# Kernel optimization log

Hardware: AMD Instinct MI355X
Metric: run time of the kernel (lower is better)

Reference implementation:

```python
import jax, jax.numpy as jnp
import numpy as np

N_NODES = 100000
N_EDGES = 1200000
N_GRAPHS = 128
IN_C, HID_C, OUT_C = 64, 128, 16


def setup_inputs() -> dict:
    key = jax.random.key(0)
    ks = jax.random.split(key, 6)
    x = jax.random.normal(ks[0], (N_NODES, IN_C), dtype=jnp.float32)
    edge_index = jax.random.randint(ks[1], (2, N_EDGES), 0, N_NODES, dtype=jnp.int64)
    batch = jnp.sort(jax.random.randint(ks[2], (N_NODES,), 0, N_GRAPHS, dtype=jnp.int64))
    W1 = jax.random.normal(ks[3], (IN_C, HID_C), dtype=jnp.float32) * (1.0 / np.sqrt(IN_C))
    b1 = jnp.zeros((HID_C,), jnp.float32)
    W2 = jax.random.normal(ks[4], (HID_C, OUT_C), dtype=jnp.float32) * (1.0 / np.sqrt(HID_C))
    b2 = jnp.zeros((OUT_C,), jnp.float32)
    return {"x": x, "edge_index": edge_index, "batch": batch,
            "W1": W1, "b1": b1, "W2": W2, "b2": b2}


def gcn_conv(x, src, dst, W, b, n):
    """PyG GCNConv: add self-loops, symmetric deg^{-1/2} normalization, scatter-add."""
    h = x @ W                                   # [n, out] dense transform first
    loop = jnp.arange(n, dtype=src.dtype)
    s = jnp.concatenate([src, loop])            # edges + self-loops
    d = jnp.concatenate([dst, loop])
    deg = jax.ops.segment_sum(jnp.ones(d.shape[0], h.dtype), d, num_segments=n)
    dinv = jnp.where(deg > 0, jax.lax.rsqrt(deg), jnp.zeros((), h.dtype))
    norm = dinv[s] * dinv[d]                    # [E + n]
    msg = h[s] * norm[:, None]                  # gather + scale
    return jax.ops.segment_sum(msg, d, num_segments=n) + b  # scatter-add


def reference(x, edge_index, batch, W1, b1, W2, b2):
    n = x.shape[0]
    src, dst = edge_index[0], edge_index[1]
    h = jax.nn.relu(gcn_conv(x, src, dst, W1, b1, n))
    h = gcn_conv(h, src, dst, W2, b2, n)
    # global_mean_pool over batch ids
    sums = jax.ops.segment_sum(h, batch, num_segments=N_GRAPHS)
    cnts = jax.ops.segment_sum(jnp.ones((n,), h.dtype), batch, num_segments=N_GRAPHS)
    pooled = sums / jnp.maximum(cnts, 1.0)[:, None]   # [N_GRAPHS, OUT_C]
    return jax.nn.log_softmax(pooled, axis=1)
```

## Files before the change

kernel.cpp:

```cpp
#include <hip/hip_runtime.h>
#include <hip/hip_bf16.h>


#define THREADS 256
#define NPB 256
#define BSTRIDE 4096
#define CH 4096
#define NBMAX 512

typedef __attribute__((ext_vector_type(8))) short bf16x8;
typedef __attribute__((ext_vector_type(4))) float f32x4;

__device__ __forceinline__ float bfu_lo(unsigned int u) {
    union { unsigned int i; float f; } v; v.i = u << 16; return v.f;
}
__device__ __forceinline__ float bfu_hi(unsigned int u) {
    union { unsigned int i; float f; } v; v.i = u & 0xffff0000u; return v.f;
}
__device__ __forceinline__ unsigned short f2bf(float f) {
    union { float f; unsigned int i; } v; v.f = f;
    unsigned int r = v.i + 0x7fff + ((v.i >> 16) & 1);
    return (unsigned short)(r >> 16);
}
__device__ __forceinline__ unsigned int packbf(float lo, float hi) {
    return (unsigned int)f2bf(lo) | ((unsigned int)f2bf(hi) << 16);
}
__device__ __forceinline__ void unpack8(uint4 u, float* f) {
    f[0] = bfu_lo(u.x); f[1] = bfu_hi(u.x);
    f[2] = bfu_lo(u.y); f[3] = bfu_hi(u.y);
    f[4] = bfu_lo(u.z); f[5] = bfu_hi(u.z);
    f[6] = bfu_lo(u.w); f[7] = bfu_hi(u.w);
}

__global__ __launch_bounds__(THREADS) void k_partition(const int* __restrict__ src,
                                                       const int* __restrict__ dst,
                                                       int* __restrict__ bucketCursor,
                                                       unsigned int* __restrict__ ebuf,
                                                       int E, int NB) {
    __shared__ int h[NBMAX];
    __shared__ int base[NBMAX];
    __shared__ int cnt[NBMAX];
    for (int b = threadIdx.x; b < NBMAX; b += THREADS) { h[b] = 0; cnt[b] = 0; }
    __syncthreads();
    int b0 = blockIdx.x * CH;
    for (int k = 0; k < CH; k += THREADS) {
        int e = b0 + k + threadIdx.x;
        if (e < E) atomicAdd(&h[dst[e] >> 8], 1);
    }
    __syncthreads();
    for (int b = threadIdx.x; b < NB; b += THREADS)
        if (h[b]) base[b] = b * BSTRIDE + atomicAdd(&bucketCursor[b], h[b]);
    __syncthreads();
    for (int k = 0; k < CH; k += THREADS) {
        int e = b0 + k + threadIdx.x;
        if (e < E) {
            int s = src[e], d = dst[e];
            int b = d >> 8;
            int i = base[b] + atomicAdd(&cnt[b], 1);
            ebuf[i] = ((unsigned int)(d & (NPB - 1)) << 17) | (unsigned int)s;
        }
    }
}

__global__ __launch_bounds__(THREADS) void k_bucket_csr(const unsigned int* __restrict__ ebuf,
                                                        const int* __restrict__ bucketCursor,
                                                        const float* __restrict__ x,
                                                        int* __restrict__ offs,
                                                        int* __restrict__ deg,
                                                        int* __restrict__ srcs,
                                                        float* __restrict__ dinv,
                                                        uint4* __restrict__ xnb,
                                                        int n) {
    __shared__ unsigned int eL[BSTRIDE];
    __shared__ int c[NPB];
    __shared__ int cur[NPB];
    __shared__ float dloc[NPB];
    __shared__ int sh[THREADS];
    const int tid = threadIdx.x;
    const int b = blockIdx.x;
    const int nbase = b * NPB;
    const int w0 = b * BSTRIDE;
    const int cnt_b = bucketCursor[b];
    c[tid] = 0;
    __syncthreads();
    for (int i = tid; i < cnt_b; i += THREADS) {
        unsigned int e = ebuf[w0 + i];
        eL[i] = e;
        atomicAdd(&c[e >> 17], 1);
    }
    __syncthreads();
    int c0 = c[tid];
    sh[tid] = c0;
    __syncthreads();
    for (int step = 1; step < THREADS; step <<= 1) {
        int t = (tid >= step) ? sh[tid - step] : 0;
        __syncthreads();
        sh[tid] += t;
        __syncthreads();
    }
    int excl = sh[tid] - c0;
    int node = nbase + tid;
    float dv = rsqrtf((float)(c0 + 1));
    dloc[tid] = dv;
    if (node < n) {
        offs[node] = w0 + excl;
        deg[node] = c0;
        dinv[node] = dv;
    }
    cur[tid] = excl;
    __syncthreads();
    for (int i = tid; i < cnt_b; i += THREADS) {
        unsigned int e = eL[i];
        int pos = w0 + atomicAdd(&cur[e >> 17], 1);
        srcs[pos] = (int)(e & 0x1FFFFu);
    }
    const float4* X4 = (const float4*)x;
    for (int i = tid; i < NPB * 8; i += THREADS) {
        int ln = i >> 3;
        int node2 = nbase + ln;
        if (node2 >= n) break;
        int q = i & 7;
        float dd = dloc[ln];
        float4 a = X4[(size_t)node2 * 16 + q * 2];
        float4 bb = X4[(size_t)node2 * 16 + q * 2 + 1];
        uint4 o;
        o.x = packbf(a.x * dd, a.y * dd);
        o.y = packbf(a.z * dd, a.w * dd);
        o.z = packbf(bb.x * dd, bb.y * dd);
        o.w = packbf(bb.z * dd, bb.w * dd);
        xnb[(size_t)node2 * 8 + q] = o;
    }
}

__global__ __launch_bounds__(THREADS) void k_gather1(const int* __restrict__ offs,
                                                     const int* __restrict__ deg,
                                                     const int* __restrict__ srcs,
                                                     const float* __restrict__ dinv,
                                                     const uint4* __restrict__ xnb,
                                                     uint4* __restrict__ aggb, int n) {
    int idx = blockIdx.x * THREADS + threadIdx.x;
    int node = idx >> 3;
    if (node >= n) return;
    int q = idx & 7;
    float acc[8];
    unpack8(xnb[(size_t)node * 8 + q], acc);
    int e0 = offs[node], e1 = e0 + deg[node];
    for (int e = e0; e < e1; ++e) {
        int s = srcs[e];
        float t[8];
        unpack8(xnb[(size_t)s * 8 + q], t);
#pragma unroll
        for (int j = 0; j < 8; ++j) acc[j] += t[j];
    }
    float dd = dinv[node];
    uint4 o;
    o.x = packbf(acc[0] * dd, acc[1] * dd);
    o.y = packbf(acc[2] * dd, acc[3] * dd);
    o.z = packbf(acc[4] * dd, acc[5] * dd);
    o.w = packbf(acc[6] * dd, acc[7] * dd);
    aggb[(size_t)node * 8 + q] = o;
}

__global__ __launch_bounds__(THREADS) void k_gemm12m(const unsigned short* __restrict__ aggb,
                                                     const float* __restrict__ W1,
                                                     const float* __restrict__ b1,
                                                     const float* __restrict__ W2,
                                                     const float* __restrict__ dinv,
                                                     unsigned short* __restrict__ ts,
                                                     int n, int ntiles) {
    __shared__ unsigned short h1L[4][16][136];
    const int wave = threadIdx.x >> 6;
    const int lane = threadIdx.x & 63;
    const int col = lane & 15;
    const int ko = lane >> 4;

    bf16x8 bfr1[2][8];
#pragma unroll
    for (int ks = 0; ks < 2; ++ks)
#pragma unroll
        for (int nt = 0; nt < 8; ++nt) {
            bf16x8 b;
#pragma unroll
            for (int j = 0; j < 8; ++j)
                b[j] = (short)f2bf(W1[(ks * 32 + ko * 8 + j) * 128 + nt * 16 + col]);
            bfr1[ks][nt] = b;
        }
    float bias[8];
#pragma unroll
    for (int nt = 0; nt < 8; ++nt) bias[nt] = b1[nt * 16 + col];
    bf16x8 bfr2[4];
#pragma unroll
    for (int ks = 0; ks < 4; ++ks) {
        bf16x8 b;
#pragma unroll
        for (int j = 0; j < 8; ++j)
            b[j] = (short)f2bf(W2[(ks * 32 + ko * 8 + j) * 16 + col]);
        bfr2[ks] = b;
    }

    const int tile0 = (blockIdx.x * 4 + wave) * 4;
    for (int t = 0; t < 4; ++t) {
        int tile = tile0 + t;
        if (tile >= ntiles) return;
        int r0 = tile * 16;
        int rowA = r0 + col;
        if (rowA >= n) rowA = n - 1;
        const bf16x8* Ap = (const bf16x8*)(aggb + (size_t)rowA * 64 + ko * 8);
        bf16x8 a0 = Ap[0];
        bf16x8 a1 = Ap[4];
        f32x4 acc[8];
#pragma unroll
        for (int nt = 0; nt < 8; ++nt) acc[nt] = (f32x4){0.f, 0.f, 0.f, 0.f};
#pragma unroll
        for (int nt = 0; nt < 8; ++nt) {
            acc[nt] = __builtin_amdgcn_mfma_f32_16x16x32_bf16(a0, bfr1[0][nt], acc[nt], 0, 0, 0);
            acc[nt] = __builtin_amdgcn_mfma_f32_16x16x32_bf16(a1, bfr1[1][nt], acc[nt], 0, 0, 0);
        }
#pragma unroll
        for (int nt = 0; nt < 8; ++nt)
#pragma unroll
            for (int r = 0; r < 4; ++r)
                h1L[wave][ko * 4 + r][nt * 16 + col] = f2bf(fmaxf(acc[nt][r] + bias[nt], 0.f));
        f32x4 acc2 = (f32x4){0.f, 0.f, 0.f, 0.f};
#pragma unroll
        for (int ks = 0; ks < 4; ++ks) {
            bf16x8 a2 = *(const bf16x8*)&h1L[wave][col][ks * 32 + ko * 8];
            acc2 = __builtin_amdgcn_mfma_f32_16x16x32_bf16(a2, bfr2[ks], acc2, 0, 0, 0);
        }
#pragma unroll
        for (int r = 0; r < 4; ++r) {
            int row = r0 + ko * 4 + r;
            if (row < n) {
                float dd = dinv[row];
                ts[(size_t)row * 16 + col] = f2bf(acc2[r] * dd);
            }
        }
    }
}

__global__ __launch_bounds__(THREADS) void k_gather2(const int* __restrict__ offs,
                                                     const int* __restrict__ deg,
                                                     const int* __restrict__ srcs,
                                                     const float* __restrict__ dinv,
                                                     const uint4* __restrict__ ts,
                                                     float* __restrict__ h2, int n) {
    int idx = blockIdx.x * THREADS + threadIdx.x;
    int node = idx >> 1;
    if (node >= n) return;
    int q = idx & 1;
    float acc[8];
    unpack8(ts[(size_t)node * 2 + q], acc);
    int e0 = offs[node], e1 = e0 + deg[node];
    for (int e = e0; e < e1; ++e) {
        int s = srcs[e];
        float t[8];
        unpack8(ts[(size_t)s * 2 + q], t);
#pragma unroll
        for (int j = 0; j < 8; ++j) acc[j] += t[j];
    }
    float dd = dinv[node];
    float4 o0 = {acc[0] * dd, acc[1] * dd, acc[2] * dd, acc[3] * dd};
    float4 o1 = {acc[4] * dd, acc[5] * dd, acc[6] * dd, acc[7] * dd};
    float4* O = (float4*)(h2 + (size_t)node * 16 + q * 8);
    O[0] = o0;
    O[1] = o1;
}

__global__ __launch_bounds__(THREADS) void k_poolfinal(const float* __restrict__ h2,
                                                       const int* __restrict__ batch,
                                                       const float* __restrict__ b2,
                                                       float* __restrict__ out, int n) {
    int g = blockIdx.x;
    int lo = 0, hi = n;
    while (lo < hi) { int mid = (lo + hi) >> 1; if (batch[mid] < g) lo = mid + 1; else hi = mid; }
    int s0 = lo;
    hi = n;
    while (lo < hi) { int mid = (lo + hi) >> 1; if (batch[mid] < g + 1) lo = mid + 1; else hi = mid; }
    int s1 = lo;

    int c = threadIdx.x & 15;
    int rg = threadIdx.x >> 4;
    float acc = 0.f;
    for (int i = s0 + rg; i < s1; i += 16) acc += h2[(size_t)i * 16 + c];
    __shared__ float red[THREADS];
    red[threadIdx.x] = acc;
    __syncthreads();
    for (int step = 128; step >= 16; step >>= 1) {
        if (threadIdx.x < step) red[threadIdx.x] += red[threadIdx.x + step];
        __syncthreads();
    }
    if (threadIdx.x == 0) {
        float cnt = fmaxf((float)(s1 - s0), 1.0f);
        float v[16];
        float mx = -1e30f;
#pragma unroll
        for (int k = 0; k < 16; ++k) {
            v[k] = red[k] / cnt + b2[k];
            mx = fmaxf(mx, v[k]);
        }
        float se = 0.f;
#pragma unroll
        for (int k = 0; k < 16; ++k) se += expf(v[k] - mx);
        float lse = logf(se) + mx;
#pragma unroll
        for (int k = 0; k < 16; ++k) out[g * 16 + k] = v[k] - lse;
    }
}

extern "C" void kernel_launch(void* const* d_in, const int* in_sizes, int n_in,
                              void* d_out, int out_size, void* d_ws, size_t ws_size,
                              hipStream_t stream) {
    const float* x    = (const float*)d_in[0];
    const int* edges  = (const int*)d_in[1];
    const int* batch  = (const int*)d_in[2];
    const float* W1   = (const float*)d_in[3];
    const float* b1   = (const float*)d_in[4];
    const float* W2   = (const float*)d_in[5];
    const float* b2   = (const float*)d_in[6];
    float* out        = (float*)d_out;

    const int n = in_sizes[2];
    const int E = in_sizes[1] / 2;
    const int* src = edges;
    const int* dst = edges + E;
    const int NB = (n + NPB - 1) / NPB;
    const int npart = (E + CH - 1) / CH;
    const int ntiles = (n + 15) / 16;

    char* ws = (char*)d_ws;
    size_t off = 0;
    auto carve = [&](size_t bytes) { char* p = ws + off; off = (off + bytes + 255) & ~(size_t)255; return p; };
    int*   bucketCursor = (int*)carve(NBMAX * 4);
    int*   offs    = (int*)carve((size_t)n * 4);
    int*   deg     = (int*)carve((size_t)n * 4);
    int*   srcs    = (int*)carve((size_t)NB * BSTRIDE * 4);
    float* dinv    = (float*)carve((size_t)n * 4);
    uint4* xnb     = (uint4*)carve((size_t)n * 64 * 2);
    char*  aggreg  = (char*)carve((size_t)n * 64 * 2);
    char*  big     = (char*)carve((size_t)NB * BSTRIDE * 4 > (size_t)n * 128 * 2
                                  ? (size_t)NB * BSTRIDE * 4 : (size_t)n * 128 * 2);
    unsigned int* ebuf = (unsigned int*)big;
    unsigned short* ts = (unsigned short*)big;
    unsigned short* aggb = (unsigned short*)aggreg;
    float* h2 = (float*)(aggreg + (size_t)n * 16 * 4);

    auto blks = [](long long work) { return (int)((work + THREADS - 1) / THREADS); };

    hipMemsetAsync(bucketCursor, 0, NBMAX * 4, stream);
    k_partition  <<<npart, THREADS, 0, stream>>>(src, dst, bucketCursor, ebuf, E, NB);
    k_bucket_csr <<<NB, THREADS, 0, stream>>>(ebuf, bucketCursor, x, offs, deg, srcs, dinv, xnb, n);

    k_gather1 <<<blks((long long)n * 8), THREADS, 0, stream>>>(offs, deg, srcs, dinv, xnb, (uint4*)aggb, n);
    k_gemm12m <<<(ntiles + 15) / 16, THREADS, 0, stream>>>(aggb, W1, b1, W2, dinv, ts, n, ntiles);
    k_gather2 <<<blks((long long)n * 2), THREADS, 0, stream>>>(offs, deg, srcs, dinv, (const uint4*)ts, h2, n);

    k_poolfinal <<<128, THREADS, 0, stream>>>(h2, batch, b2, out, n);
}
```

Baseline: 132.6 us.

## Fuse second-layer gather with mean pooling via shared-memory atomics; cache dst in LDS

The second GCN aggregation now pools directly into per-graph sums. Each block accumulates into a shared-memory table with atomics and then flushes it to global sums, so the per-node h2 array is never written or re-read, and a tiny single-block kernel does the normalisation and log-softmax. The partition kernel also keeps dst values in LDS so they are read from global memory only once. This costs shared-memory atomic contention and global float atomics, which make the summation order nondeterministic.

```diff
diff --git a/kernel.cpp b/kernel.cpp
--- a/kernel.cpp
+++ b/kernel.cpp
@@ -7,6 +7,7 @@
 #define BSTRIDE 4096
 #define CH 4096
 #define NBMAX 512
+#define NGRAPH 128
 
 typedef __attribute__((ext_vector_type(8))) short bf16x8;
 typedef __attribute__((ext_vector_type(4))) float f32x4;
@@ -40,12 +41,17 @@
     __shared__ int h[NBMAX];
     __shared__ int base[NBMAX];
     __shared__ int cnt[NBMAX];
+    __shared__ int dL[CH];
     for (int b = threadIdx.x; b < NBMAX; b += THREADS) { h[b] = 0; cnt[b] = 0; }
     __syncthreads();
     int b0 = blockIdx.x * CH;
     for (int k = 0; k < CH; k += THREADS) {
         int e = b0 + k + threadIdx.x;
-        if (e < E) atomicAdd(&h[dst[e] >> 8], 1);
+        if (e < E) {
+            int d = dst[e];
+            dL[k + threadIdx.x] = d;
+            atomicAdd(&h[d >> 8], 1);
+        }
     }
     __syncthreads();
     for (int b = threadIdx.x; b < NB; b += THREADS)
@@ -54,7 +60,8 @@
     for (int k = 0; k < CH; k += THREADS) {
         int e = b0 + k + threadIdx.x;
         if (e < E) {
-            int s = src[e], d = dst[e];
+            int s = src[e];
+            int d = dL[k + threadIdx.x];
             int b = d >> 8;
             int i = base[b] + atomicAdd(&cnt[b], 1);
             ebuf[i] = ((unsigned int)(d & (NPB - 1)) << 17) | (unsigned int)s;
@@ -238,73 +245,69 @@
     }
 }
 
-__global__ __launch_bounds__(THREADS) void k_gather2(const int* __restrict__ offs,
-                                                     const int* __restrict__ deg,
-                                                     const int* __restrict__ srcs,
-                                                     const float* __restrict__ dinv,
-                                                     const uint4* __restrict__ ts,
-                                                     float* __restrict__ h2, int n) {
-    int idx = blockIdx.x * THREADS + threadIdx.x;
+__global__ __launch_bounds__(THREADS) void k_gatherpool(const int* __restrict__ offs,
+                                                        const int* __restrict__ deg,
+                                                        const int* __restrict__ srcs,
+                                                        const float* __restrict__ dinv,
+                                                        const uint4* __restrict__ ts,
+                                                        const int* __restrict__ batch,
+                                                        float* __restrict__ sums, int n) {
+    __shared__ float gsum[NGRAPH * 16];
+    const int tid = threadIdx.x;
+    for (int i = tid; i < NGRAPH * 16; i += THREADS) gsum[i] = 0.f;
+    __syncthreads();
+    int idx = blockIdx.x * THREADS + tid;
     int node = idx >> 1;
-    if (node >= n) return;
-    int q = idx & 1;
-    float acc[8];
-    unpack8(ts[(size_t)node * 2 + q], acc);
-    int e0 = offs[node], e1 = e0 + deg[node];
-    for (int e = e0; e < e1; ++e) {
-        int s = srcs[e];
-        float t[8];
-        unpack8(ts[(size_t)s * 2 + q], t);
-#pragma unroll
-        for (int j = 0; j < 8; ++j) acc[j] += t[j];
-    }
-    float dd = dinv[node];
-    float4 o0 = {acc[0] * dd, acc[1] * dd, acc[2] * dd, acc[3] * dd};
-    float4 o1 = {acc[4] * dd, acc[5] * dd, acc[6] * dd, acc[7] * dd};
-    float4* O = (float4*)(h2 + (size_t)node * 16 + q * 8);
-    O[0] = o0;
-    O[1] = o1;
-}
-
-__global__ __launch_bounds__(THREADS) void k_poolfinal(const float* __restrict__ h2,
-                                                       const int* __restrict__ batch,
-                                                       const float* __restrict__ b2,
-                                                       float* __restrict__ out, int n) {
-    int g = blockIdx.x;
+    if (node < n) {
+        int q = idx & 1;
+        float acc[8];
+        unpack8(ts[(size_t)node * 2 + q], acc);
+        int e0 = offs[node], e1 = e0 + deg[node];
+        for (int e = e0; e < e1; ++e) {
+            int s = srcs[e];
+            float t[8];
+            unpack8(ts[(size_t)s * 2 + q], t);
+#pragma unroll
+            for (int j = 0; j < 8; ++j) acc[j] += t[j];
+        }
+        float dd = dinv[node];
+        int g = batch[node];
+        float* row = &gsum[g * 16 + q * 8];
+#pragma unroll
+        for (int j = 0; j < 8; ++j) atomicAdd(&row[j], acc[j] * dd);
+    }
+    __syncthreads();
+    for (int i = tid; i < NGRAPH * 16; i += THREADS) {
+        float v = gsum[i];
+        if (v != 0.f) atomicAdd(&sums[i], v);
+    }
+}
+
+__global__ __launch_bounds__(NGRAPH) void k_final(const float* __restrict__ sums,
+                                                  const int* __restrict__ batch,
+                                                  const float* __restrict__ b2,
+                                                  float* __restrict__ out, int n) {
+    int g = threadIdx.x;
     int lo = 0, hi = n;
     while (lo < hi) { int mid = (lo + hi) >> 1; if (batch[mid] < g) lo = mid + 1; else hi = mid; }
     int s0 = lo;
     hi = n;
     while (lo < hi) { int mid = (lo + hi) >> 1; if (batch[mid] < g + 1) lo = mid + 1; else hi = mid; }
     int s1 = lo;
-
-    int c = threadIdx.x & 15;
-    int rg = threadIdx.x >> 4;
-    float acc = 0.f;
-    for (int i = s0 + rg; i < s1; i += 16) acc += h2[(size_t)i * 16 + c];
-    __shared__ float red[THREADS];
-    red[threadIdx.x] = acc;
-    __syncthreads();
-    for (int step = 128; step >= 16; step >>= 1) {
-        if (threadIdx.x < step) red[threadIdx.x] += red[threadIdx.x + step];
-        __syncthreads();
-    }
-    if (threadIdx.x == 0) {
-        float cnt = fmaxf((float)(s1 - s0), 1.0f);
-        float v[16];
-        float mx = -1e30f;
-#pragma unroll
-        for (int k = 0; k < 16; ++k) {
-            v[k] = red[k] / cnt + b2[k];
-            mx = fmaxf(mx, v[k]);
-        }
-        float se = 0.f;
-#pragma unroll
-        for (int k = 0; k < 16; ++k) se += expf(v[k] - mx);
-        float lse = logf(se) + mx;
-#pragma unroll
-        for (int k = 0; k < 16; ++k) out[g * 16 + k] = v[k] - lse;
-    }
+    float cnt = fmaxf((float)(s1 - s0), 1.0f);
+    float v[16];
+    float mx = -1e30f;
+#pragma unroll
+    for (int c = 0; c < 16; ++c) {
+        v[c] = sums[g * 16 + c] / cnt + b2[c];
+        mx = fmaxf(mx, v[c]);
+    }
+    float se = 0.f;
+#pragma unroll
+    for (int c = 0; c < 16; ++c) se += expf(v[c] - mx);
+    float lse = logf(se) + mx;
+#pragma unroll
+    for (int c = 0; c < 16; ++c) out[g * 16 + c] = v[c] - lse;
 }
 
 extern "C" void kernel_launch(void* const* d_in, const int* in_sizes, int n_in,
@@ -331,6 +334,7 @@
     size_t off = 0;
     auto carve = [&](size_t bytes) { char* p = ws + off; off = (off + bytes + 255) & ~(size_t)255; return p; };
     int*   bucketCursor = (int*)carve(NBMAX * 4);
+    float* sums    = (float*)carve(NGRAPH * 16 * 4);
     int*   offs    = (int*)carve((size_t)n * 4);
     int*   deg     = (int*)carve((size_t)n * 4);
     int*   srcs    = (int*)carve((size_t)NB * BSTRIDE * 4);
@@ -342,17 +346,17 @@
     unsigned int* ebuf = (unsigned int*)big;
     unsigned short* ts = (unsigned short*)big;
     unsigned short* aggb = (unsigned short*)aggreg;
-    float* h2 = (float*)(aggreg + (size_t)n * 16 * 4);
 
     auto blks = [](long long work) { return (int)((work + THREADS - 1) / THREADS); };
 
-    hipMemsetAsync(bucketCursor, 0, NBMAX * 4, stream);
+    hipMemsetAsync(bucketCursor, 0, NBMAX * 4 + NGRAPH * 16 * 4, stream);
     k_partition  <<<npart, THREADS, 0, stream>>>(src, dst, bucketCursor, ebuf, E, NB);
     k_bucket_csr <<<NB, THREADS, 0, stream>>>(ebuf, bucketCursor, x, offs, deg, srcs, dinv, xnb, n);
 
     k_gather1 <<<blks((long long)n * 8), THREADS, 0, stream>>>(offs, deg, srcs, dinv, xnb, (uint4*)aggb, n);
     k_gemm12m <<<(ntiles + 15) / 16, THREADS, 0, stream>>>(aggb, W1, b1, W2, dinv, ts, n, ntiles);
-    k_gather2 <<<blks((long long)n * 2), THREADS, 0, stream>>>(offs, deg, srcs, dinv, (const uint4*)ts, h2, n);
-
-    k_poolfinal <<<128, THREADS, 0, stream>>>(h2, batch, b2, out, n);
-}
+
+    k_gatherpool <<<blks((long long)n * 2), THREADS, 0, stream>>>(offs, deg, srcs, dinv,
+                                                                  (const uint4*)ts, batch, sums, n);
+    k_final <<<1, NGRAPH, 0, stream>>>(sums, batch, b2, out, n);
+}
```

After: 129.0 us. 2.7% less time.
